# Performance work log

Hardware: AMD Instinct MI355X
Metric: run time of the kernel (lower is better)

Reference implementation:

```python
import jax, jax.numpy as jnp
import numpy as np

LEAK = 0.9
BASE_THRESH = 1.0
BN_EPS = 1e-5

@jax.custom_vjp
def spike_fn(x):
    return (x >= 0).astype(x.dtype)

def _spike_fwd(x):
    return (x >= 0).astype(x.dtype), x

def _spike_bwd(x, g):
    return (g / (1.0 + 5.0 * jnp.abs(x)) ** 2,)

spike_fn.defvjp(_spike_fwd, _spike_bwd)


def setup_inputs() -> dict:
    key = jax.random.key(0)
    ks = jax.random.split(key, 8)
    B, T, C, H, NC, DT = 256, 2048, 64, 64, 4, 50
    kin_spikes_seq = jax.random.normal(ks[0], (B, T, C), dtype=jnp.float32)
    tda_features = jax.random.normal(ks[1], (B, DT), dtype=jnp.float32)
    # spatial_conv1x1: Linear(64 -> 64, bias=False); weight [out, in]
    W_spatial = jax.random.normal(ks[2], (H, C), dtype=jnp.float32) / np.sqrt(C)
    bn_gamma = jnp.ones((H,), dtype=jnp.float32)
    bn_beta = jnp.zeros((H,), dtype=jnp.float32)
    # class_conv1x1: Linear(64 -> 4, bias=False)
    W_class = jax.random.normal(ks[3], (NC, H), dtype=jnp.float32) / np.sqrt(H)
    lateral = jnp.eye(NC, dtype=jnp.float32) * 0.8 - 0.1
    # tda_to_thresh: Linear(50 -> 4)
    W_tda = jax.random.normal(ks[4], (NC, DT), dtype=jnp.float32) / np.sqrt(DT)
    b_tda = jnp.zeros((NC,), dtype=jnp.float32)
    return {
        "kin_spikes_seq": kin_spikes_seq,
        "tda_features": tda_features,
        "W_spatial": W_spatial,
        "bn_gamma": bn_gamma,
        "bn_beta": bn_beta,
        "W_class": W_class,
        "lateral": lateral,
        "W_tda": W_tda,
        "b_tda": b_tda,
    }


def reference(kin_spikes_seq, tda_features, W_spatial, bn_gamma, bn_beta,
              W_class, lateral, W_tda, b_tda):
    # [B, T, C] @ [C, H] -> [B, T, H]
    x_proj = jnp.einsum("btc,hc->bth", kin_spikes_seq, W_spatial)
    # BatchNorm1d in training mode: per-channel stats over (B, T)
    mean = jnp.mean(x_proj, axis=(0, 1))
    var = jnp.var(x_proj, axis=(0, 1))
    x_proj = (x_proj - mean) * jax.lax.rsqrt(var + BN_EPS) * bn_gamma + bn_beta

    tda_mod = jax.nn.sigmoid(tda_features @ W_tda.T + b_tda) * 0.5  # [B, 4]
    dynamic_thresh = BASE_THRESH + tda_mod

    B = kin_spikes_seq.shape[0]
    H, NC = W_class.shape[1], W_class.shape[0]
    mem1 = jnp.zeros((B, H), dtype=x_proj.dtype)
    mem2 = jnp.zeros((B, NC), dtype=x_proj.dtype)
    spike_sum = jnp.zeros((B, NC), dtype=x_proj.dtype)

    def step(carry, xt):
        mem1, mem2, ssum = carry
        mem1 = LEAK * mem1 + xt
        spk1 = spike_fn(mem1 - BASE_THRESH)
        mem1 = mem1 * (1.0 - spk1)
        cur2 = (spk1 @ W_class.T) @ lateral  # [B, 4]
        mem2 = LEAK * mem2 + cur2
        spk2 = spike_fn(mem2 - dynamic_thresh)
        mem2 = mem2 * (1.0 - spk2)
        return (mem1, mem2, ssum + spk2), None

    xs = jnp.swapaxes(x_proj, 0, 1)  # [T, B, H]
    (mem1, mem2, spike_sum), _ = jax.lax.scan(step, (mem1, mem2, spike_sum), xs)
    return spike_sum
```

## Files before the change

### kernel.cpp

```cpp
#include <hip/hip_runtime.h>
#include <cstdint>
#include <cstddef>

#define BB 256
#define TB 2048
#define NROWS (BB*TB)
#define R1 128
#define NBLK1 (NROWS/R1)

typedef float f32x4 __attribute__((ext_vector_type(4)));

#define OFF_X      0ull
#define SZ_X       ((size_t)NROWS*64*4)
#define OFF_PART   (OFF_X + SZ_X)
#define SZ_PART    ((size_t)128*NBLK1*4)
#define OFF_STAT   (OFF_PART + SZ_PART)
#define SZ_STAT    (128*8)
#define OFF_PARAM  (OFF_STAT + SZ_STAT)
#define SZ_PARAM   ((size_t)(64+64+1024)*4)
#define OFF_MASK   ((OFF_PARAM + SZ_PARAM + 255ull) & ~255ull)
#define SZ_MASK    ((size_t)NROWS*8)
#define OFF_CUR2   (OFF_MASK + SZ_MASK)
#define SZ_CUR2    ((size_t)NROWS*4*4)

__global__ __launch_bounds__(128, 2) void k1_gemm(const float* __restrict__ kin,
                                                  const float* __restrict__ Wsp,
                                                  float* __restrict__ xproj,
                                                  float* __restrict__ partials) {
  __shared__ float4 As[R1 * 16];
  __shared__ float4 Ws4[64 * 16];
  const int tid = threadIdx.x;
  const size_t r0 = (size_t)blockIdx.x * R1;

  const f32x4* kin4 = (const f32x4*)(kin + r0 * 64);
  #pragma unroll
  for (int k = 0; k < 16; ++k) {
    int idx = k * 128 + tid;
    int r = idx >> 4, cc = idx & 15;
    f32x4 v = __builtin_nontemporal_load(&kin4[idx]);
    As[r * 16 + (cc ^ ((r >> 2) & 7))] = make_float4(v.x, v.y, v.z, v.w);
  }
  const float4* W4 = (const float4*)Wsp;
  #pragma unroll
  for (int k = 0; k < 8; ++k) {
    int idx = k * 128 + tid;
    int h = idx >> 4, cc = idx & 15;
    Ws4[h * 16 + (cc ^ ((h >> 2) & 7))] = W4[idx];
  }
  __syncthreads();

  const int ty = tid >> 3;
  const int tx = tid & 7;
  float acc[8][8];
  #pragma unroll
  for (int i = 0; i < 8; ++i)
    #pragma unroll
    for (int j = 0; j < 8; ++j) acc[i][j] = 0.f;

  #pragma unroll 1
  for (int cc = 0; cc < 16; ++cc) {
    float4 av[8], wv[8];
    #pragma unroll
    for (int i = 0; i < 8; ++i)
      av[i] = As[(8 * ty + i) * 16 + (cc ^ ((2 * ty + (i >> 2)) & 7))];
    #pragma unroll
    for (int j = 0; j < 8; ++j)
      wv[j] = Ws4[(8 * tx + j) * 16 + (cc ^ ((2 * tx + (j >> 2)) & 7))];
    #pragma unroll
    for (int i = 0; i < 8; ++i)
      #pragma unroll
      for (int j = 0; j < 8; ++j) {
        acc[i][j] = fmaf(av[i].x, wv[j].x, acc[i][j]);
        acc[i][j] = fmaf(av[i].y, wv[j].y, acc[i][j]);
        acc[i][j] = fmaf(av[i].z, wv[j].z, acc[i][j]);
        acc[i][j] = fmaf(av[i].w, wv[j].w, acc[i][j]);
      }
  }

  #pragma unroll
  for (int i = 0; i < 8; ++i) {
    const size_t row = r0 + 8 * ty + i;
    *(float4*)(xproj + row * 64 + 8 * tx) =
        make_float4(acc[i][0], acc[i][1], acc[i][2], acc[i][3]);
    *(float4*)(xproj + row * 64 + 8 * tx + 4) =
        make_float4(acc[i][4], acc[i][5], acc[i][6], acc[i][7]);
  }

  __syncthreads();
  float* Sm = (float*)As;
  float* Sq = Sm + 64 * 17;
  #pragma unroll
  for (int j = 0; j < 8; ++j) {
    const int col = 8 * tx + j;
    float s = 0.f, q = 0.f;
    #pragma unroll
    for (int i = 0; i < 8; ++i) {
      s += acc[i][j];
      q += acc[i][j] * acc[i][j];
    }
    Sm[col * 17 + ty] = s;
    Sq[col * 17 + ty] = q;
  }
  __syncthreads();
  if (tid < 64) {
    float s = 0.f, q = 0.f;
    #pragma unroll
    for (int g = 0; g < 16; ++g) {
      s += Sm[tid * 17 + g];
      q += Sq[tid * 17 + g];
    }
    partials[(size_t)tid * NBLK1 + blockIdx.x]        = s;
    partials[(size_t)(64 + tid) * NBLK1 + blockIdx.x] = q;
  }
}

__global__ __launch_bounds__(256) void k2a_reduce(const float* __restrict__ partials,
                                                  double* __restrict__ statd) {
  __shared__ double sd[256];
  const int idx = blockIdx.x;
  double acc = 0.0;
  for (int k = threadIdx.x; k < NBLK1; k += 256)
    acc += (double)partials[(size_t)idx * NBLK1 + k];
  sd[threadIdx.x] = acc;
  __syncthreads();
  for (int s = 128; s > 0; s >>= 1) {
    if (threadIdx.x < s) sd[threadIdx.x] += sd[threadIdx.x + s];
    __syncthreads();
  }
  if (threadIdx.x == 0) statd[idx] = sd[0];
}

__global__ __launch_bounds__(256) void k2b_final(const double* __restrict__ statd,
                                                 const float* __restrict__ gamma,
                                                 const float* __restrict__ beta,
                                                 const float* __restrict__ tda,
                                                 const float* __restrict__ Wtda,
                                                 const float* __restrict__ btda,
                                                 float* __restrict__ param) {
  const int tid = threadIdx.x;
  if (tid < 64) {
    double mean = statd[tid] / (double)NROWS;
    double ex2  = statd[64 + tid] / (double)NROWS;
    double var  = ex2 - mean * mean;
    double sc   = (double)gamma[tid] / sqrt(var + 1e-5);
    param[tid]      = (float)sc;
    param[64 + tid] = (float)((double)beta[tid] - mean * sc);
  }
  const int b = tid;
  #pragma unroll
  for (int j = 0; j < 4; ++j) {
    double acc = (double)btda[j];
    for (int k = 0; k < 50; ++k)
      acc += (double)tda[b * 50 + k] * (double)Wtda[j * 50 + k];
    double sig = 1.0 / (1.0 + exp(-acc));
    param[128 + b * 4 + j] = (float)(1.0 + 0.5 * sig);
  }
}

#define K3_LOAD(BUF, TBASE)                         \
  { _Pragma("unroll") for (int i_ = 0; i_ < 64; ++i_) \
      BUF[i_] = xr[(size_t)((TBASE) + i_) * 64]; }

#define K3_CHUNK(CUR, NXT0, TBASE)                                   \
  { unsigned long long keep = 0;                                     \
    _Pragma("unroll") for (int i_ = 0; i_ < 64; ++i_) {              \
      bool sp = (mem >= 1.0f);                                       \
      unsigned long long mb = __ballot(sp);                          \
      if (h == i_) keep = mb;                                        \
      float xrn = (i_ < 63) ? CUR[(i_ + 1) & 63] : (NXT0);           \
      float xn = fmaf(xrn, sc, sh);                                  \
      mem = sp ? xn : fmaf(mem, 0.9f, xn);                           \
    }                                                                \
    masksB[(size_t)b * TB + (TBASE) + h] = keep; }

__global__ __launch_bounds__(64) void k3_scan1(const float* __restrict__ xproj,
                                               const float* __restrict__ param,
                                               unsigned long long* __restrict__ masksB) {
  const int b = blockIdx.x, h = threadIdx.x;
  const float sc = param[h], sh = param[64 + h];
  const float* xr = xproj + (size_t)b * TB * 64 + h;
  float xa[64], xb[64];

  K3_LOAD(xa, 0)
  float mem = fmaf(xa[0], sc, sh);

  #pragma unroll 1
  for (int t0 = 0; t0 < TB; t0 += 128) {
    K3_LOAD(xb, t0 + 64)
    K3_CHUNK(xa, xb[0], t0)
    if (t0 + 128 < TB) { K3_LOAD(xa, t0 + 128) }
    K3_CHUNK(xb, xa[0], t0 + 64)
  }
}

__global__ __launch_bounds__(256) void k4_cur2(const unsigned long long* __restrict__ masksB,
                                               const float* __restrict__ Wc,
                                               const float* __restrict__ lat,
                                               float* __restrict__ cur2T) {
  __shared__ float WcL[256];
  __shared__ float latL[16];
  const int tid = threadIdx.x, b = blockIdx.x;
  WcL[tid] = Wc[tid];
  if (tid < 16) latL[tid] = lat[tid];
  __syncthreads();

  #pragma unroll 1
  for (int c = 0; c < 8; ++c) {
    const int t = c * 256 + tid;
    const unsigned long long m = masksB[(size_t)b * TB + t];
    const unsigned lo = (unsigned)m, hi = (unsigned)(m >> 32);
    float v0 = 0.f, v1 = 0.f, v2 = 0.f, v3 = 0.f;
    #pragma unroll
    for (int hh = 0; hh < 32; ++hh) {
      const float bit = (float)((lo >> hh) & 1u);
      v0 = fmaf(bit, WcL[hh],       v0);
      v1 = fmaf(bit, WcL[64 + hh],  v1);
      v2 = fmaf(bit, WcL[128 + hh], v2);
      v3 = fmaf(bit, WcL[192 + hh], v3);
    }
    #pragma unroll
    for (int hh = 32; hh < 64; ++hh) {
      const float bit = (float)((hi >> (hh - 32)) & 1u);
      v0 = fmaf(bit, WcL[hh],       v0);
      v1 = fmaf(bit, WcL[64 + hh],  v1);
      v2 = fmaf(bit, WcL[128 + hh], v2);
      v3 = fmaf(bit, WcL[192 + hh], v3);
    }
    float o0, o1, o2, o3;
    { float cx = v0 * latL[0];  cx = fmaf(v1, latL[4],  cx); cx = fmaf(v2, latL[8],  cx); cx = fmaf(v3, latL[12], cx); o0 = cx; }
    { float cx = v0 * latL[1];  cx = fmaf(v1, latL[5],  cx); cx = fmaf(v2, latL[9],  cx); cx = fmaf(v3, latL[13], cx); o1 = cx; }
    { float cx = v0 * latL[2];  cx = fmaf(v1, latL[6],  cx); cx = fmaf(v2, latL[10], cx); cx = fmaf(v3, latL[14], cx); o2 = cx; }
    { float cx = v0 * latL[3];  cx = fmaf(v1, latL[7],  cx); cx = fmaf(v2, latL[11], cx); cx = fmaf(v3, latL[15], cx); o3 = cx; }
    cur2T[(size_t)(b * 4 + 0) * TB + t] = o0;
    cur2T[(size_t)(b * 4 + 1) * TB + t] = o1;
    cur2T[(size_t)(b * 4 + 2) * TB + t] = o2;
    cur2T[(size_t)(b * 4 + 3) * TB + t] = o3;
  }
}

#define K5_LOAD(BUF, TBASE)                                              \
  { _Pragma("unroll") for (int k_ = 0; k_ < 16; ++k_) {                  \
      float4 v = cr[((TBASE) >> 2) + k_];                                \
      BUF[4 * k_] = v.x; BUF[4 * k_ + 1] = v.y;                          \
      BUF[4 * k_ + 2] = v.z; BUF[4 * k_ + 3] = v.w; } }

#define K5_CHUNK(CUR, NXT0)                                   \
  { _Pragma("unroll") for (int i_ = 0; i_ < 64; ++i_) {       \
      bool sp = (mem >= th);                                  \
      cnt += sp ? 1u : 0u;                                    \
      float xn = (i_ < 63) ? CUR[(i_ + 1) & 63] : (NXT0);     \
      mem = sp ? xn : fmaf(mem, 0.9f, xn);                    \
    } }

__global__ __launch_bounds__(64) void k5_scan2(const float* __restrict__ cur2T,
                                               const float* __restrict__ param,
                                               float* __restrict__ out) {
  const int g = blockIdx.x * 64 + threadIdx.x;
  const float th = param[128 + g];
  const float4* cr = (const float4*)(cur2T + (size_t)g * TB);
  float ca[64], cb[64];

  K5_LOAD(ca, 0)
  float mem = ca[0];
  unsigned cnt = 0;

  #pragma unroll 1
  for (int t0 = 0; t0 < TB; t0 += 128) {
    K5_LOAD(cb, t0 + 64)
    K5_CHUNK(ca, cb[0])
    if (t0 + 128 < TB) { K5_LOAD(ca, t0 + 128) }
    K5_CHUNK(cb, ca[0])
  }
  out[g] = (float)cnt;
}

extern "C" void kernel_launch(void* const* d_in, const int* in_sizes, int n_in,
                              void* d_out, int out_size, void* d_ws, size_t ws_size,
                              hipStream_t stream) {
  const float* kin   = (const float*)d_in[0];
  const float* tda   = (const float*)d_in[1];
  const float* Wsp   = (const float*)d_in[2];
  const float* gamma = (const float*)d_in[3];
  const float* beta  = (const float*)d_in[4];
  const float* Wc    = (const float*)d_in[5];
  const float* lat   = (const float*)d_in[6];
  const float* Wtda  = (const float*)d_in[7];
  const float* btda  = (const float*)d_in[8];

  char* ws = (char*)d_ws;
  float*  xproj    = (float*)(ws + OFF_X);
  float*  partials = (float*)(ws + OFF_PART);
  double* statd    = (double*)(ws + OFF_STAT);
  float*  param    = (float*)(ws + OFF_PARAM);
  unsigned long long* masksB = (unsigned long long*)(ws + OFF_MASK);
  float*  cur2T    = (float*)(ws + OFF_CUR2);
  float*  out      = (float*)d_out;

  k1_gemm  <<<dim3(NBLK1), dim3(128), 0, stream>>>(kin, Wsp, xproj, partials);
  k2a_reduce<<<dim3(128),  dim3(256), 0, stream>>>(partials, statd);
  k2b_final<<<dim3(1),     dim3(256), 0, stream>>>(statd, gamma, beta, tda, Wtda, btda, param);
  k3_scan1 <<<dim3(BB),    dim3(64),  0, stream>>>(xproj, param, masksB);
  k4_cur2  <<<dim3(BB),    dim3(256), 0, stream>>>(masksB, Wc, lat, cur2T);
  k5_scan2 <<<dim3(16),    dim3(64),  0, stream>>>(cur2T, param, out);
}
```

Before: 178.4 us.

## Enlarge GEMM blocks, parallelize TDA threshold, spread second scan over more CUs

The projection GEMM now handles 256 rows per block with 256 threads. The LDS swizzle is adjusted to match, and each block writes two partial-stat slots so the reduction layout stays the same. The TDA threshold computation is spread over 4 blocks with one thread per (batch, class) output, instead of a serial per-thread loop inside a single block. The class-level scan runs one wave per batch element across 256 blocks instead of 16 blocks, so each CU runs fewer serial scans. The cost is 16x redundant lanes per wave in the final scan and higher LDS use per GEMM block, which may lower occupancy.

```diff
diff --git a/kernel.cpp b/kernel.cpp
--- a/kernel.cpp
+++ b/kernel.cpp
@@ -5,8 +5,9 @@
 #define BB 256
 #define TB 2048
 #define NROWS (BB*TB)
-#define R1 128
-#define NBLK1 (NROWS/R1)
+#define R1 256
+#define NBLK_K1 (NROWS/R1)
+#define NBLK1 4096
 
 typedef float f32x4 __attribute__((ext_vector_type(4)));
 
@@ -23,7 +24,7 @@
 #define OFF_CUR2   (OFF_MASK + SZ_MASK)
 #define SZ_CUR2    ((size_t)NROWS*4*4)
 
-__global__ __launch_bounds__(128, 2) void k1_gemm(const float* __restrict__ kin,
+__global__ __launch_bounds__(256, 2) void k1_gemm(const float* __restrict__ kin,
                                                   const float* __restrict__ Wsp,
                                                   float* __restrict__ xproj,
                                                   float* __restrict__ partials) {
@@ -35,17 +36,17 @@
   const f32x4* kin4 = (const f32x4*)(kin + r0 * 64);
   #pragma unroll
   for (int k = 0; k < 16; ++k) {
-    int idx = k * 128 + tid;
+    int idx = k * 256 + tid;
     int r = idx >> 4, cc = idx & 15;
     f32x4 v = __builtin_nontemporal_load(&kin4[idx]);
-    As[r * 16 + (cc ^ ((r >> 2) & 7))] = make_float4(v.x, v.y, v.z, v.w);
+    As[r * 16 + (cc ^ ((r >> 3) & 7))] = make_float4(v.x, v.y, v.z, v.w);
   }
   const float4* W4 = (const float4*)Wsp;
   #pragma unroll
-  for (int k = 0; k < 8; ++k) {
-    int idx = k * 128 + tid;
+  for (int k = 0; k < 4; ++k) {
+    int idx = k * 256 + tid;
     int h = idx >> 4, cc = idx & 15;
-    Ws4[h * 16 + (cc ^ ((h >> 2) & 7))] = W4[idx];
+    Ws4[h * 16 + (cc ^ ((h >> 3) & 7))] = W4[idx];
   }
   __syncthreads();
 
@@ -62,10 +63,10 @@
     float4 av[8], wv[8];
     #pragma unroll
     for (int i = 0; i < 8; ++i)
-      av[i] = As[(8 * ty + i) * 16 + (cc ^ ((2 * ty + (i >> 2)) & 7))];
+      av[i] = As[(8 * ty + i) * 16 + (cc ^ (ty & 7))];
     #pragma unroll
     for (int j = 0; j < 8; ++j)
-      wv[j] = Ws4[(8 * tx + j) * 16 + (cc ^ ((2 * tx + (j >> 2)) & 7))];
+      wv[j] = Ws4[(8 * tx + j) * 16 + (cc ^ tx)];
     #pragma unroll
     for (int i = 0; i < 8; ++i)
       #pragma unroll
@@ -88,7 +89,7 @@
 
   __syncthreads();
   float* Sm = (float*)As;
-  float* Sq = Sm + 64 * 17;
+  float* Sq = Sm + 64 * 33;
   #pragma unroll
   for (int j = 0; j < 8; ++j) {
     const int col = 8 * tx + j;
@@ -98,19 +99,21 @@
       s += acc[i][j];
       q += acc[i][j] * acc[i][j];
     }
-    Sm[col * 17 + ty] = s;
-    Sq[col * 17 + ty] = q;
+    Sm[col * 33 + ty] = s;
+    Sq[col * 33 + ty] = q;
   }
   __syncthreads();
   if (tid < 64) {
-    float s = 0.f, q = 0.f;
-    #pragma unroll
-    for (int g = 0; g < 16; ++g) {
-      s += Sm[tid * 17 + g];
-      q += Sq[tid * 17 + g];
-    }
-    partials[(size_t)tid * NBLK1 + blockIdx.x]        = s;
-    partials[(size_t)(64 + tid) * NBLK1 + blockIdx.x] = q;
+    float s0 = 0.f, q0 = 0.f, s1 = 0.f, q1 = 0.f;
+    #pragma unroll
+    for (int g = 0; g < 16; ++g)  { s0 += Sm[tid * 33 + g]; q0 += Sq[tid * 33 + g]; }
+    #pragma unroll
+    for (int g = 16; g < 32; ++g) { s1 += Sm[tid * 33 + g]; q1 += Sq[tid * 33 + g]; }
+    const size_t p0 = 2 * (size_t)blockIdx.x;
+    partials[(size_t)tid * NBLK1 + p0]            = s0;
+    partials[(size_t)tid * NBLK1 + p0 + 1]        = s1;
+    partials[(size_t)(64 + tid) * NBLK1 + p0]     = q0;
+    partials[(size_t)(64 + tid) * NBLK1 + p0 + 1] = q1;
   }
 }
 
@@ -137,24 +140,25 @@
                                                  const float* __restrict__ Wtda,
                                                  const float* __restrict__ btda,
                                                  float* __restrict__ param) {
-  const int tid = threadIdx.x;
-  if (tid < 64) {
-    double mean = statd[tid] / (double)NROWS;
-    double ex2  = statd[64 + tid] / (double)NROWS;
-    double var  = ex2 - mean * mean;
-    double sc   = (double)gamma[tid] / sqrt(var + 1e-5);
-    param[tid]      = (float)sc;
-    param[64 + tid] = (float)((double)beta[tid] - mean * sc);
-  }
-  const int b = tid;
-  #pragma unroll
-  for (int j = 0; j < 4; ++j) {
-    double acc = (double)btda[j];
-    for (int k = 0; k < 50; ++k)
-      acc += (double)tda[b * 50 + k] * (double)Wtda[j * 50 + k];
-    double sig = 1.0 / (1.0 + exp(-acc));
-    param[128 + b * 4 + j] = (float)(1.0 + 0.5 * sig);
-  }
+  const int tid = threadIdx.x, blk = blockIdx.x;
+  if (blk == 4) {
+    if (tid < 64) {
+      double mean = statd[tid] / (double)NROWS;
+      double ex2  = statd[64 + tid] / (double)NROWS;
+      double var  = ex2 - mean * mean;
+      double sc   = (double)gamma[tid] / sqrt(var + 1e-5);
+      param[tid]      = (float)sc;
+      param[64 + tid] = (float)((double)beta[tid] - mean * sc);
+    }
+    return;
+  }
+  const int g = blk * 256 + tid;
+  const int b = g >> 2, j = g & 3;
+  double acc = (double)btda[j];
+  for (int k = 0; k < 50; ++k)
+    acc += (double)tda[b * 50 + k] * (double)Wtda[j * 50 + k];
+  double sig = 1.0 / (1.0 + exp(-acc));
+  param[128 + g] = (float)(1.0 + 0.5 * sig);
 }
 
 #define K3_LOAD(BUF, TBASE)                         \
@@ -255,7 +259,9 @@
 __global__ __launch_bounds__(64) void k5_scan2(const float* __restrict__ cur2T,
                                                const float* __restrict__ param,
                                                float* __restrict__ out) {
-  const int g = blockIdx.x * 64 + threadIdx.x;
+  const int b = blockIdx.x;
+  const int j4 = threadIdx.x & 3;
+  const int g = b * 4 + j4;
   const float th = param[128 + g];
   const float4* cr = (const float4*)(cur2T + (size_t)g * TB);
   float ca[64], cb[64];
@@ -271,7 +277,7 @@
     if (t0 + 128 < TB) { K5_LOAD(ca, t0 + 128) }
     K5_CHUNK(cb, ca[0])
   }
-  out[g] = (float)cnt;
+  if (threadIdx.x < 4) out[g] = (float)cnt;
 }
 
 extern "C" void kernel_launch(void* const* d_in, const int* in_sizes, int n_in,
@@ -296,10 +302,10 @@
   float*  cur2T    = (float*)(ws + OFF_CUR2);
   float*  out      = (float*)d_out;
 
-  k1_gemm  <<<dim3(NBLK1), dim3(128), 0, stream>>>(kin, Wsp, xproj, partials);
+  k1_gemm  <<<dim3(NBLK_K1), dim3(256), 0, stream>>>(kin, Wsp, xproj, partials);
   k2a_reduce<<<dim3(128),  dim3(256), 0, stream>>>(partials, statd);
-  k2b_final<<<dim3(1),     dim3(256), 0, stream>>>(statd, gamma, beta, tda, Wtda, btda, param);
+  k2b_final<<<dim3(5),     dim3(256), 0, stream>>>(statd, gamma, beta, tda, Wtda, btda, param);
   k3_scan1 <<<dim3(BB),    dim3(64),  0, stream>>>(xproj, param, masksB);
   k4_cur2  <<<dim3(BB),    dim3(256), 0, stream>>>(masksB, Wc, lat, cur2T);
-  k5_scan2 <<<dim3(16),    dim3(64),  0, stream>>>(cur2T, param, out);
-}
+  k5_scan2 <<<dim3(BB),    dim3(64),  0, stream>>>(cur2T, param, out);
+}
```

New measurement: 163.7 us. 8.3% less time.
